# Performance work log

Measured on AMD Instinct MI355X. Metric: run time of the kernel, lower is better.

The kernel has to match this reference:

```python
import jax, jax.numpy as jnp
import numpy as np

N_NODES = 100000
N_EDGES = 1600000
D_IN = 64
D_HID = 64
D_ACT = 16


def gcn_conv(x, W, b, src, dst, n_nodes):
    """PyG-style GCNConv: D^-1/2 (A+I) D^-1/2 (x @ W) + b."""
    h = x @ W  # [N, out]
    ones = jnp.ones(src.shape[0], dtype=x.dtype)
    # degree with self-loops (in-degree + 1)
    deg = jax.ops.segment_sum(ones, dst, num_segments=n_nodes) + 1.0
    dinv = jax.lax.rsqrt(deg)  # [N]
    coef = dinv[src] * dinv[dst]  # [E]
    agg = jax.ops.segment_sum(h[src] * coef[:, None], dst, num_segments=n_nodes)
    agg = agg + h * (dinv * dinv)[:, None]  # self-loop term
    return agg + b


def setup_inputs() -> dict:
    key = jax.random.key(0)
    ks = jax.random.split(key, 6)
    x = jax.random.normal(ks[0], (N_NODES, D_IN), dtype=jnp.float32)
    edge_index = jax.random.randint(ks[1], (2, N_EDGES), 0, N_NODES, dtype=jnp.int64)
    s1 = 1.0 / np.sqrt(D_IN)
    s2 = 1.0 / np.sqrt(D_HID)
    W1 = jax.random.normal(ks[2], (D_IN, D_HID), dtype=jnp.float32) * s1
    b1 = jnp.zeros((D_HID,), dtype=jnp.float32)
    W2 = jax.random.normal(ks[3], (D_HID, D_HID), dtype=jnp.float32) * s2
    b2 = jnp.zeros((D_HID,), dtype=jnp.float32)
    Wfc = jax.random.normal(ks[4], (D_HID, D_ACT), dtype=jnp.float32) * s2
    bfc = jnp.zeros((D_ACT,), dtype=jnp.float32)
    return {"x": x, "edge_index": edge_index, "W1": W1, "b1": b1,
            "W2": W2, "b2": b2, "Wfc": Wfc, "bfc": bfc}


def reference(x, edge_index, W1, b1, W2, b2, Wfc, bfc):
    src, dst = edge_index[0], edge_index[1]
    n = x.shape[0]
    h = jax.nn.relu(gcn_conv(x, W1, b1, src, dst, n))
    h = jax.nn.relu(gcn_conv(h, W2, b2, src, dst, n))
    q_values = h @ Wfc + bfc
    return q_values
```

## Files before the change

### kernel.cpp

```cpp
#include <hip/hip_runtime.h>

#define NN 100000
#define NE 1600000
#define NCAP 64
#define NB2 782
#define NBP2 1024
#define CAP2 2560
#define CHUNK 2048
#define NCHUNK 782

typedef __attribute__((ext_vector_type(8))) short short8;
typedef __attribute__((ext_vector_type(4))) float f32x4;

static __device__ __forceinline__ unsigned short f2bf(float f) {
    unsigned u = __float_as_uint(f);
    u += 0x7fffu + ((u >> 16) & 1u);
    return (unsigned short)(u >> 16);
}
static __device__ __forceinline__ float bflo(unsigned u) { return __uint_as_float(u << 16); }
static __device__ __forceinline__ float bfhi(unsigned u) { return __uint_as_float(u & 0xffff0000u); }

static __device__ __forceinline__ short8 as_s8(uint4 u) {
    union { uint4 u4; short8 s8; } x; x.u4 = u; return x.s8;
}
static __device__ __forceinline__ f32x4 mfma16(short8 a, short8 b, f32x4 c) {
    return __builtin_amdgcn_mfma_f32_16x16x32_bf16(a, b, c, 0, 0, 0);
}

static __device__ __forceinline__ void split8(float4 a, float4 b, short8& hi8, short8& lo8) {
    float vv[8] = {a.x, a.y, a.z, a.w, b.x, b.y, b.z, b.w};
    unsigned h[8], l[8];
    #pragma unroll
    for (int j = 0; j < 8; ++j) {
        h[j] = f2bf(vv[j]);
        l[j] = f2bf(vv[j] - bflo(h[j]));
    }
    uint4 uh, ul;
    uh.x = h[0] | (h[1] << 16); uh.y = h[2] | (h[3] << 16);
    uh.z = h[4] | (h[5] << 16); uh.w = h[6] | (h[7] << 16);
    ul.x = l[0] | (l[1] << 16); ul.y = l[2] | (l[3] << 16);
    ul.z = l[4] | (l[5] << 16); ul.w = l[6] | (l[7] << 16);
    hi8 = as_s8(uh); lo8 = as_s8(ul);
}

__global__ void zero_gcur(int* __restrict__ p) {
    int t = blockIdx.x * blockDim.x + threadIdx.x;
    if (t < NBP2) p[t] = 0;
}

__global__ __launch_bounds__(256) void bin_edges(const int* __restrict__ src,
                                                 const int* __restrict__ dst,
                                                 int* __restrict__ gcur,
                                                 int* __restrict__ pairs) {
    __shared__ int lcnt[NBP2];
    __shared__ int lnext[NBP2];
    int t = threadIdx.x;
    #pragma unroll
    for (int i = 0; i < 4; ++i) lcnt[t + 256 * i] = 0;
    __syncthreads();
    int base = blockIdx.x * CHUNK;
    int end = min(base + CHUNK, NE);
    for (int e = base + t; e < end; e += 256) atomicAdd(&lcnt[dst[e] >> 7], 1);
    __syncthreads();
    #pragma unroll
    for (int i = 0; i < 4; ++i) {
        int b = t + 256 * i;
        int v = lcnt[b];
        if (v) lnext[b] = b * CAP2 + atomicAdd(&gcur[b], v);
    }
    __syncthreads();
    for (int e = base + t; e < end; e += 256) {
        int d = dst[e];
        int p = atomicAdd(&lnext[d >> 7], 1);
        pairs[p] = src[e] | ((d & 127) << 17);
    }
}

__global__ __launch_bounds__(256) void slab_place(const int* __restrict__ pairs,
                                                  const int* __restrict__ gcur,
                                                  int* __restrict__ esrc,
                                                  int* __restrict__ cnt,
                                                  float* __restrict__ dinv) {
    __shared__ int lc[128];
    int b = blockIdx.x;
    int t = threadIdx.x;
    if (t < 128) lc[t] = 0;
    __syncthreads();
    int e0 = b * CAP2;
    int e1 = e0 + min(gcur[b], CAP2);
    for (int i = e0 + t; i < e1; i += 256) {
        int w = pairs[i];
        int li = w >> 17;
        int p = atomicAdd(&lc[li], 1);
        if (p < NCAP) esrc[(((b << 7) + li) << 6) + p] = w & 0x1FFFF;
    }
    __syncthreads();
    if (t < 128) {
        int node = (b << 7) + t;
        if (node < NN) {
            int c = lc[t];
            cnt[node] = min(c, NCAP);
            dinv[node] = rsqrtf((float)c + 1.0f);
        }
    }
}

__global__ void wpack(const float* __restrict__ W1, const float* __restrict__ W2,
                      uint4* __restrict__ P) {
    int tid = blockIdx.x * blockDim.x + threadIdx.x;
    if (tid >= 1024) return;
    int w = tid >> 9;
    int f = tid & 511;
    int c = f >> 7;
    int t = (f >> 6) & 1;
    int lane = f & 63;
    const float* W = w ? W2 : W1;
    int k0 = t * 32 + (lane >> 4) * 8;
    int n  = c * 16 + (lane & 15);
    unsigned sh[8], sl[8];
    #pragma unroll
    for (int j = 0; j < 8; ++j) {
        float v = W[(k0 + j) * 64 + n];
        sh[j] = f2bf(v);
        sl[j] = f2bf(v - bflo(sh[j]));
    }
    uint4 ph, pl;
    ph.x = sh[0] | (sh[1] << 16); ph.y = sh[2] | (sh[3] << 16);
    ph.z = sh[4] | (sh[5] << 16); ph.w = sh[6] | (sh[7] << 16);
    pl.x = sl[0] | (sl[1] << 16); pl.y = sl[2] | (sl[3] << 16);
    pl.z = sl[4] | (sl[5] << 16); pl.w = sl[6] | (sl[7] << 16);
    P[w * 1024 + f]       = ph;
    P[w * 1024 + 512 + f] = pl;
}

__global__ __launch_bounds__(256) void gemm1_mfma(const float* __restrict__ X,
                                                  const uint4* __restrict__ WP,
                                                  const float* __restrict__ dinv,
                                                  uint4* __restrict__ G4) {
    __shared__ __align__(16) unsigned short Ls[4][16][64];
    int wave = threadIdx.x >> 6, lane = threadIdx.x & 63;
    int tile = blockIdx.x * 4 + wave;
    bool active = tile < (NN / 16);
    int node0 = (active ? tile : 0) * 16;
    int r = lane & 15, g = lane >> 4;

    const float* xr = X + (size_t)(node0 + r) * 64 + g * 8;
    float4 x0a = *(const float4*)(xr);
    float4 x0b = *(const float4*)(xr + 4);
    float4 x1a = *(const float4*)(xr + 32);
    float4 x1b = *(const float4*)(xr + 36);
    short8 ah0, al0, ah1, al1;
    split8(x0a, x0b, ah0, al0);
    split8(x1a, x1b, ah1, al1);

    f32x4 acc[4];
    #pragma unroll
    for (int c = 0; c < 4; ++c) acc[c] = (f32x4){0.f, 0.f, 0.f, 0.f};
    #pragma unroll
    for (int c = 0; c < 4; ++c) {
        short8 bh0 = as_s8(WP[(c * 2 + 0) * 64 + lane]);
        short8 bl0 = as_s8(WP[512 + (c * 2 + 0) * 64 + lane]);
        short8 bh1 = as_s8(WP[(c * 2 + 1) * 64 + lane]);
        short8 bl1 = as_s8(WP[512 + (c * 2 + 1) * 64 + lane]);
        acc[c] = mfma16(ah0, bh0, acc[c]);
        acc[c] = mfma16(al0, bh0, acc[c]);
        acc[c] = mfma16(ah0, bl0, acc[c]);
        acc[c] = mfma16(ah1, bh1, acc[c]);
        acc[c] = mfma16(al1, bh1, acc[c]);
        acc[c] = mfma16(ah1, bl1, acc[c]);
    }
    float dd[4];
    #pragma unroll
    for (int rr = 0; rr < 4; ++rr) dd[rr] = dinv[node0 + g * 4 + rr];
    #pragma unroll
    for (int c = 0; c < 4; ++c) {
        #pragma unroll
        for (int rr = 0; rr < 4; ++rr)
            Ls[wave][g * 4 + rr][c * 16 + r] = f2bf(acc[c][rr] * dd[rr]);
    }
    __syncthreads();
    if (active) {
        #pragma unroll
        for (int i = 0; i < 2; ++i) {
            int idx = lane + i * 64;
            int row = idx >> 3, u = idx & 7;
            G4[(size_t)(node0 + row) * 8 + u] = *(const uint4*)&Ls[wave][row][u * 8];
        }
    }
}

__global__ __launch_bounds__(256) void gemm2_mfma(const uint4* __restrict__ X4,
                                                  const uint4* __restrict__ WP,
                                                  const float* __restrict__ dinv,
                                                  uint4* __restrict__ G4) {
    __shared__ __align__(16) unsigned short Ls[4][16][64];
    int wave = threadIdx.x >> 6, lane = threadIdx.x & 63;
    int tile = blockIdx.x * 4 + wave;
    bool active = tile < (NN / 16);
    int node0 = (active ? tile : 0) * 16;
    int r = lane & 15, g = lane >> 4;

    short8 a0 = as_s8(X4[(size_t)(node0 + r) * 8 + g]);
    short8 a1 = as_s8(X4[(size_t)(node0 + r) * 8 + 4 + g]);

    f32x4 acc[4];
    #pragma unroll
    for (int c = 0; c < 4; ++c) acc[c] = (f32x4){0.f, 0.f, 0.f, 0.f};
    #pragma unroll
    for (int c = 0; c < 4; ++c) {
        short8 bh0 = as_s8(WP[(c * 2 + 0) * 64 + lane]);
        short8 bl0 = as_s8(WP[512 + (c * 2 + 0) * 64 + lane]);
        short8 bh1 = as_s8(WP[(c * 2 + 1) * 64 + lane]);
        short8 bl1 = as_s8(WP[512 + (c * 2 + 1) * 64 + lane]);
        acc[c] = mfma16(a0, bh0, acc[c]);
        acc[c] = mfma16(a0, bl0, acc[c]);
        acc[c] = mfma16(a1, bh1, acc[c]);
        acc[c] = mfma16(a1, bl1, acc[c]);
    }
    float dd[4];
    #pragma unroll
    for (int rr = 0; rr < 4; ++rr) dd[rr] = dinv[node0 + g * 4 + rr];
    #pragma unroll
    for (int c = 0; c < 4; ++c) {
        #pragma unroll
        for (int rr = 0; rr < 4; ++rr)
            Ls[wave][g * 4 + rr][c * 16 + r] = f2bf(acc[c][rr] * dd[rr]);
    }
    __syncthreads();
    if (active) {
        #pragma unroll
        for (int i = 0; i < 2; ++i) {
            int idx = lane + i * 64;
            int row = idx >> 3, u = idx & 7;
            G4[(size_t)(node0 + row) * 8 + u] = *(const uint4*)&Ls[wave][row][u * 8];
        }
    }
}

__global__ __launch_bounds__(256) void gather_bf16(
        const int* __restrict__ cnt, const int* __restrict__ esrc,
        const float* __restrict__ dinv, const uint4* __restrict__ G4,
        const float* __restrict__ b, uint4* __restrict__ outH) {
    int node = (int)((blockIdx.x * blockDim.x + threadIdx.x) >> 6);
    int lane = threadIdx.x & 63;
    int e = lane >> 3, m = lane & 7;
    int j0 = node << 6;
    int e1 = j0 + cnt[node];
    float a0 = 0.f, a1 = 0.f, a2 = 0.f, a3 = 0.f, a4 = 0.f, a5 = 0.f, a6 = 0.f, a7 = 0.f;
    int j = j0 + e;
    for (; j + 8 < e1; j += 16) {
        int s0 = esrc[j], s1 = esrc[j + 8];
        uint4 u0 = G4[s0 * 8 + m];
        uint4 u1 = G4[s1 * 8 + m];
        a0 += bflo(u0.x) + bflo(u1.x); a1 += bfhi(u0.x) + bfhi(u1.x);
        a2 += bflo(u0.y) + bflo(u1.y); a3 += bfhi(u0.y) + bfhi(u1.y);
        a4 += bflo(u0.z) + bflo(u1.z); a5 += bfhi(u0.z) + bfhi(u1.z);
        a6 += bflo(u0.w) + bflo(u1.w); a7 += bfhi(u0.w) + bfhi(u1.w);
    }
    for (; j < e1; j += 8) {
        uint4 u = G4[esrc[j] * 8 + m];
        a0 += bflo(u.x); a1 += bfhi(u.x); a2 += bflo(u.y); a3 += bfhi(u.y);
        a4 += bflo(u.z); a5 += bfhi(u.z); a6 += bflo(u.w); a7 += bfhi(u.w);
    }
    a0 += __shfl_xor(a0, 8);  a1 += __shfl_xor(a1, 8);  a2 += __shfl_xor(a2, 8);  a3 += __shfl_xor(a3, 8);
    a4 += __shfl_xor(a4, 8);  a5 += __shfl_xor(a5, 8);  a6 += __shfl_xor(a6, 8);  a7 += __shfl_xor(a7, 8);
    a0 += __shfl_xor(a0, 16); a1 += __shfl_xor(a1, 16); a2 += __shfl_xor(a2, 16); a3 += __shfl_xor(a3, 16);
    a4 += __shfl_xor(a4, 16); a5 += __shfl_xor(a5, 16); a6 += __shfl_xor(a6, 16); a7 += __shfl_xor(a7, 16);
    a0 += __shfl_xor(a0, 32); a1 += __shfl_xor(a1, 32); a2 += __shfl_xor(a2, 32); a3 += __shfl_xor(a3, 32);
    a4 += __shfl_xor(a4, 32); a5 += __shfl_xor(a5, 32); a6 += __shfl_xor(a6, 32); a7 += __shfl_xor(a7, 32);
    if (e == 0) {
        float dd = dinv[node];
        uint4 us = G4[node * 8 + m];
        a0 += bflo(us.x); a1 += bfhi(us.x); a2 += bflo(us.y); a3 += bfhi(us.y);
        a4 += bflo(us.z); a5 += bfhi(us.z); a6 += bflo(us.w); a7 += bfhi(us.w);
        float4 b0 = ((const float4*)b)[2 * m];
        float4 b1v = ((const float4*)b)[2 * m + 1];
        float h0 = fmaxf(fmaf(a0, dd, b0.x), 0.f);
        float h1 = fmaxf(fmaf(a1, dd, b0.y), 0.f);
        float h2 = fmaxf(fmaf(a2, dd, b0.z), 0.f);
        float h3 = fmaxf(fmaf(a3, dd, b0.w), 0.f);
        float h4 = fmaxf(fmaf(a4, dd, b1v.x), 0.f);
        float h5 = fmaxf(fmaf(a5, dd, b1v.y), 0.f);
        float h6 = fmaxf(fmaf(a6, dd, b1v.z), 0.f);
        float h7 = fmaxf(fmaf(a7, dd, b1v.w), 0.f);
        uint4 pk;
        pk.x = (unsigned)f2bf(h0) | ((unsigned)f2bf(h1) << 16);
        pk.y = (unsigned)f2bf(h2) | ((unsigned)f2bf(h3) << 16);
        pk.z = (unsigned)f2bf(h4) | ((unsigned)f2bf(h5) << 16);
        pk.w = (unsigned)f2bf(h6) | ((unsigned)f2bf(h7) << 16);
        outH[(size_t)node * 8 + m] = pk;
    }
}

__global__ __launch_bounds__(256) void gather_fc(
        const int* __restrict__ cnt, const int* __restrict__ esrc,
        const float* __restrict__ dinv, const uint4* __restrict__ G4,
        const float* __restrict__ b2, const float* __restrict__ Wfc,
        const float* __restrict__ bfc, float* __restrict__ out) {
    int tid = threadIdx.x;
    int w = tid >> 6, lane = tid & 63;
    int e = lane >> 3, m = lane & 7;
    int q = lane >> 4, c = lane & 15;
    int node = blockIdx.x * 4 + w;
    float Wreg[16];
    #pragma unroll
    for (int i = 0; i < 16; ++i) Wreg[i] = Wfc[(q * 16 + i) * 16 + c];
    int j0 = node << 6;
    int e1 = j0 + cnt[node];
    float a0 = 0.f, a1 = 0.f, a2 = 0.f, a3 = 0.f, a4 = 0.f, a5 = 0.f, a6 = 0.f, a7 = 0.f;
    int j = j0 + e;
    for (; j + 8 < e1; j += 16) {
        int s0 = esrc[j], s1 = esrc[j + 8];
        uint4 u0 = G4[s0 * 8 + m];
        uint4 u1 = G4[s1 * 8 + m];
        a0 += bflo(u0.x) + bflo(u1.x); a1 += bfhi(u0.x) + bfhi(u1.x);
        a2 += bflo(u0.y) + bflo(u1.y); a3 += bfhi(u0.y) + bfhi(u1.y);
        a4 += bflo(u0.z) + bflo(u1.z); a5 += bfhi(u0.z) + bfhi(u1.z);
        a6 += bflo(u0.w) + bflo(u1.w); a7 += bfhi(u0.w) + bfhi(u1.w);
    }
    for (; j < e1; j += 8) {
        uint4 u = G4[esrc[j] * 8 + m];
        a0 += bflo(u.x); a1 += bfhi(u.x); a2 += bflo(u.y); a3 += bfhi(u.y);
        a4 += bflo(u.z); a5 += bfhi(u.z); a6 += bflo(u.w); a7 += bfhi(u.w);
    }
    a0 += __shfl_xor(a0, 8);  a1 += __shfl_xor(a1, 8);  a2 += __shfl_xor(a2, 8);  a3 += __shfl_xor(a3, 8);
    a4 += __shfl_xor(a4, 8);  a5 += __shfl_xor(a5, 8);  a6 += __shfl_xor(a6, 8);  a7 += __shfl_xor(a7, 8);
    a0 += __shfl_xor(a0, 16); a1 += __shfl_xor(a1, 16); a2 += __shfl_xor(a2, 16); a3 += __shfl_xor(a3, 16);
    a4 += __shfl_xor(a4, 16); a5 += __shfl_xor(a5, 16); a6 += __shfl_xor(a6, 16); a7 += __shfl_xor(a7, 16);
    a0 += __shfl_xor(a0, 32); a1 += __shfl_xor(a1, 32); a2 += __shfl_xor(a2, 32); a3 += __shfl_xor(a3, 32);
    a4 += __shfl_xor(a4, 32); a5 += __shfl_xor(a5, 32); a6 += __shfl_xor(a6, 32); a7 += __shfl_xor(a7, 32);
    float dd = dinv[node];
    uint4 us = G4[node * 8 + m];
    a0 += bflo(us.x); a1 += bfhi(us.x); a2 += bflo(us.y); a3 += bfhi(us.y);
    a4 += bflo(us.z); a5 += bfhi(us.z); a6 += bflo(us.w); a7 += bfhi(us.w);
    float4 b0 = ((const float4*)b2)[2 * m];
    float4 b1v = ((const float4*)b2)[2 * m + 1];
    a0 = fmaxf(fmaf(a0, dd, b0.x), 0.f);
    a1 = fmaxf(fmaf(a1, dd, b0.y), 0.f);
    a2 = fmaxf(fmaf(a2, dd, b0.z), 0.f);
    a3 = fmaxf(fmaf(a3, dd, b0.w), 0.f);
    a4 = fmaxf(fmaf(a4, dd, b1v.x), 0.f);
    a5 = fmaxf(fmaf(a5, dd, b1v.y), 0.f);
    a6 = fmaxf(fmaf(a6, dd, b1v.z), 0.f);
    a7 = fmaxf(fmaf(a7, dd, b1v.w), 0.f);
    int sl0 = 2 * q, sl1 = 2 * q + 1;
    float acc = 0.f;
    acc = fmaf(__shfl(a0, sl0), Wreg[0], acc);
    acc = fmaf(__shfl(a1, sl0), Wreg[1], acc);
    acc = fmaf(__shfl(a2, sl0), Wreg[2], acc);
    acc = fmaf(__shfl(a3, sl0), Wreg[3], acc);
    acc = fmaf(__shfl(a4, sl0), Wreg[4], acc);
    acc = fmaf(__shfl(a5, sl0), Wreg[5], acc);
    acc = fmaf(__shfl(a6, sl0), Wreg[6], acc);
    acc = fmaf(__shfl(a7, sl0), Wreg[7], acc);
    acc = fmaf(__shfl(a0, sl1), Wreg[8], acc);
    acc = fmaf(__shfl(a1, sl1), Wreg[9], acc);
    acc = fmaf(__shfl(a2, sl1), Wreg[10], acc);
    acc = fmaf(__shfl(a3, sl1), Wreg[11], acc);
    acc = fmaf(__shfl(a4, sl1), Wreg[12], acc);
    acc = fmaf(__shfl(a5, sl1), Wreg[13], acc);
    acc = fmaf(__shfl(a6, sl1), Wreg[14], acc);
    acc = fmaf(__shfl(a7, sl1), Wreg[15], acc);
    acc += __shfl_xor(acc, 16);
    acc += __shfl_xor(acc, 32);
    if (lane < 16) out[node * 16 + c] = acc + bfc[c];
}

extern "C" void kernel_launch(void* const* d_in, const int* in_sizes, int n_in,
                              void* d_out, int out_size, void* d_ws, size_t ws_size,
                              hipStream_t stream) {
    const float* x   = (const float*)d_in[0];
    const int*   ei  = (const int*)d_in[1];
    const float* W1  = (const float*)d_in[2];
    const float* b1  = (const float*)d_in[3];
    const float* W2  = (const float*)d_in[4];
    const float* b2  = (const float*)d_in[5];
    const float* Wfc = (const float*)d_in[6];
    const float* bfc = (const float*)d_in[7];
    float* out = (float*)d_out;

    const int* src = ei;
    const int* dst = ei + NE;

    int*      gcur  = (int*)d_ws;
    int*      cnt   = gcur + NBP2;
    float*    dinvp = (float*)(cnt + NN);
    int*      esrc  = (int*)(dinvp + NN);
    unsigned* G     = (unsigned*)(esrc + (size_t)NN * NCAP);
    uint4*    bufB  = (uint4*)(G + (size_t)NN * 32);
    uint4*    WPK   = (uint4*)((unsigned*)bufB + (size_t)NN * 32);
    int*      pairs = (int*)bufB;

    zero_gcur<<<4, 256, 0, stream>>>(gcur);
    wpack<<<4, 256, 0, stream>>>(W1, W2, WPK);
    bin_edges<<<NCHUNK, 256, 0, stream>>>(src, dst, gcur, pairs);
    slab_place<<<NB2, 256, 0, stream>>>(pairs, gcur, esrc, cnt, dinvp);

    gemm1_mfma<<<(NN / 16 + 3) / 4, 256, 0, stream>>>(x, WPK, dinvp, (uint4*)G);
    gather_bf16<<<NN / 4, 256, 0, stream>>>(cnt, esrc, dinvp, (const uint4*)G, b1, bufB);

    gemm2_mfma<<<(NN / 16 + 3) / 4, 256, 0, stream>>>(bufB, WPK + 1024, dinvp, (uint4*)G);
    gather_fc<<<NN / 4, 256, 0, stream>>>(cnt, esrc, dinvp, (const uint4*)G, b2, Wfc, bfc, out);
}
```

Before: 249.7 us.

## Batch neighbor-index loads via shuffle, fuse gcur zeroing, register-cache edges in binning

The gather kernels now load all of a node's neighbor indices in one coalesced 64-lane read and broadcast them with shuffles. They then issue up to four (or eight) independent feature-row loads before accumulating, replacing the serial index-then-load loop and exposing more memory-level parallelism. Zeroing of the bin counters moves into the weight-packing kernel, which removes one launch. Binning keeps each thread's eight src/dst values in registers so the second pass does not re-read them from global memory. The costs are extra registers and predicated loads for low-degree nodes.

```diff
diff --git a/kernel.cpp b/kernel.cpp
--- a/kernel.cpp
+++ b/kernel.cpp
@@ -43,11 +43,6 @@
     hi8 = as_s8(uh); lo8 = as_s8(ul);
 }
 
-__global__ void zero_gcur(int* __restrict__ p) {
-    int t = blockIdx.x * blockDim.x + threadIdx.x;
-    if (t < NBP2) p[t] = 0;
-}
-
 __global__ __launch_bounds__(256) void bin_edges(const int* __restrict__ src,
                                                  const int* __restrict__ dst,
                                                  int* __restrict__ gcur,
@@ -59,8 +54,15 @@
     for (int i = 0; i < 4; ++i) lcnt[t + 256 * i] = 0;
     __syncthreads();
     int base = blockIdx.x * CHUNK;
-    int end = min(base + CHUNK, NE);
-    for (int e = base + t; e < end; e += 256) atomicAdd(&lcnt[dst[e] >> 7], 1);
+    int sr[8], dr[8];
+    #pragma unroll
+    for (int i = 0; i < 8; ++i) {
+        int e = base + t + 256 * i;
+        bool v = e < NE;
+        sr[i] = v ? src[e] : 0;
+        dr[i] = v ? dst[e] : -1;
+        if (v) atomicAdd(&lcnt[dr[i] >> 7], 1);
+    }
     __syncthreads();
     #pragma unroll
     for (int i = 0; i < 4; ++i) {
@@ -69,10 +71,12 @@
         if (v) lnext[b] = b * CAP2 + atomicAdd(&gcur[b], v);
     }
     __syncthreads();
-    for (int e = base + t; e < end; e += 256) {
-        int d = dst[e];
-        int p = atomicAdd(&lnext[d >> 7], 1);
-        pairs[p] = src[e] | ((d & 127) << 17);
+    #pragma unroll
+    for (int i = 0; i < 8; ++i) {
+        if (dr[i] >= 0) {
+            int p = atomicAdd(&lnext[dr[i] >> 7], 1);
+            pairs[p] = sr[i] | ((dr[i] & 127) << 17);
+        }
     }
 }
 
@@ -106,9 +110,10 @@
 }
 
 __global__ void wpack(const float* __restrict__ W1, const float* __restrict__ W2,
-                      uint4* __restrict__ P) {
+                      uint4* __restrict__ P, int* __restrict__ gcur) {
     int tid = blockIdx.x * blockDim.x + threadIdx.x;
     if (tid >= 1024) return;
+    gcur[tid] = 0;
     int w = tid >> 9;
     int f = tid & 511;
     int c = f >> 7;
@@ -237,37 +242,65 @@
     }
 }
 
+#define ACC8(u) do { \
+    a0 += bflo((u).x); a1 += bfhi((u).x); a2 += bflo((u).y); a3 += bfhi((u).y); \
+    a4 += bflo((u).z); a5 += bfhi((u).z); a6 += bflo((u).w); a7 += bfhi((u).w); } while (0)
+
+#define GATHER_CORE(node)                                                     \
+    int deg = cnt[node];                                                      \
+    int sidx = esrc[((node) << 6) + lane];                                    \
+    int nt = (deg - e + 7) >> 3;        \
+    int s0 = __shfl(sidx, e);                                                 \
+    int s1 = __shfl(sidx, e + 8);                                             \
+    int s2 = __shfl(sidx, e + 16);                                            \
+    int s3 = __shfl(sidx, e + 24);                                            \
+    float a0 = 0.f, a1 = 0.f, a2 = 0.f, a3 = 0.f,                             \
+          a4 = 0.f, a5 = 0.f, a6 = 0.f, a7 = 0.f;                             \
+    uint4 u0, u1, u2, u3;                                                     \
+    if (nt > 0) u0 = G4[s0 * 8 + m];                                          \
+    if (nt > 1) u1 = G4[s1 * 8 + m];                                          \
+    if (nt > 2) u2 = G4[s2 * 8 + m];                                          \
+    if (nt > 3) u3 = G4[s3 * 8 + m];                                          \
+    if (nt > 0) ACC8(u0);                                                     \
+    if (nt > 1) ACC8(u1);                                                     \
+    if (nt > 2) ACC8(u2);                                                     \
+    if (nt > 3) ACC8(u3);                                                     \
+    if (__any(nt > 4)) {                          \
+        int s4 = __shfl(sidx, e + 32);                                        \
+        int s5 = __shfl(sidx, e + 40);                                        \
+        int s6 = __shfl(sidx, e + 48);                                        \
+        int s7 = __shfl(sidx, e + 56);                                        \
+        uint4 u4, u5, u6, u7;                                                 \
+        if (nt > 4) u4 = G4[s4 * 8 + m];                                      \
+        if (nt > 5) u5 = G4[s5 * 8 + m];                                      \
+        if (nt > 6) u6 = G4[s6 * 8 + m];                                      \
+        if (nt > 7) u7 = G4[s7 * 8 + m];                                      \
+        if (nt > 4) ACC8(u4);                                                 \
+        if (nt > 5) ACC8(u5);                                                 \
+        if (nt > 6) ACC8(u6);                                                 \
+        if (nt > 7) ACC8(u7);                                                 \
+    }                                                                         \
+    a0 += __shfl_xor(a0, 8);  a1 += __shfl_xor(a1, 8);                        \
+    a2 += __shfl_xor(a2, 8);  a3 += __shfl_xor(a3, 8);                        \
+    a4 += __shfl_xor(a4, 8);  a5 += __shfl_xor(a5, 8);                        \
+    a6 += __shfl_xor(a6, 8);  a7 += __shfl_xor(a7, 8);                        \
+    a0 += __shfl_xor(a0, 16); a1 += __shfl_xor(a1, 16);                       \
+    a2 += __shfl_xor(a2, 16); a3 += __shfl_xor(a3, 16);                       \
+    a4 += __shfl_xor(a4, 16); a5 += __shfl_xor(a5, 16);                       \
+    a6 += __shfl_xor(a6, 16); a7 += __shfl_xor(a7, 16);                       \
+    a0 += __shfl_xor(a0, 32); a1 += __shfl_xor(a1, 32);                       \
+    a2 += __shfl_xor(a2, 32); a3 += __shfl_xor(a3, 32);                       \
+    a4 += __shfl_xor(a4, 32); a5 += __shfl_xor(a5, 32);                       \
+    a6 += __shfl_xor(a6, 32); a7 += __shfl_xor(a7, 32);
+
 __global__ __launch_bounds__(256) void gather_bf16(
         const int* __restrict__ cnt, const int* __restrict__ esrc,
         const float* __restrict__ dinv, const uint4* __restrict__ G4,
         const float* __restrict__ b, uint4* __restrict__ outH) {
-    int node = (int)((blockIdx.x * blockDim.x + threadIdx.x) >> 6);
+    int node = blockIdx.x * 4 + (threadIdx.x >> 6);
     int lane = threadIdx.x & 63;
     int e = lane >> 3, m = lane & 7;
-    int j0 = node << 6;
-    int e1 = j0 + cnt[node];
-    float a0 = 0.f, a1 = 0.f, a2 = 0.f, a3 = 0.f, a4 = 0.f, a5 = 0.f, a6 = 0.f, a7 = 0.f;
-    int j = j0 + e;
-    for (; j + 8 < e1; j += 16) {
-        int s0 = esrc[j], s1 = esrc[j + 8];
-        uint4 u0 = G4[s0 * 8 + m];
-        uint4 u1 = G4[s1 * 8 + m];
-        a0 += bflo(u0.x) + bflo(u1.x); a1 += bfhi(u0.x) + bfhi(u1.x);
-        a2 += bflo(u0.y) + bflo(u1.y); a3 += bfhi(u0.y) + bfhi(u1.y);
-        a4 += bflo(u0.z) + bflo(u1.z); a5 += bfhi(u0.z) + bfhi(u1.z);
-        a6 += bflo(u0.w) + bflo(u1.w); a7 += bfhi(u0.w) + bfhi(u1.w);
-    }
-    for (; j < e1; j += 8) {
-        uint4 u = G4[esrc[j] * 8 + m];
-        a0 += bflo(u.x); a1 += bfhi(u.x); a2 += bflo(u.y); a3 += bfhi(u.y);
-        a4 += bflo(u.z); a5 += bfhi(u.z); a6 += bflo(u.w); a7 += bfhi(u.w);
-    }
-    a0 += __shfl_xor(a0, 8);  a1 += __shfl_xor(a1, 8);  a2 += __shfl_xor(a2, 8);  a3 += __shfl_xor(a3, 8);
-    a4 += __shfl_xor(a4, 8);  a5 += __shfl_xor(a5, 8);  a6 += __shfl_xor(a6, 8);  a7 += __shfl_xor(a7, 8);
-    a0 += __shfl_xor(a0, 16); a1 += __shfl_xor(a1, 16); a2 += __shfl_xor(a2, 16); a3 += __shfl_xor(a3, 16);
-    a4 += __shfl_xor(a4, 16); a5 += __shfl_xor(a5, 16); a6 += __shfl_xor(a6, 16); a7 += __shfl_xor(a7, 16);
-    a0 += __shfl_xor(a0, 32); a1 += __shfl_xor(a1, 32); a2 += __shfl_xor(a2, 32); a3 += __shfl_xor(a3, 32);
-    a4 += __shfl_xor(a4, 32); a5 += __shfl_xor(a5, 32); a6 += __shfl_xor(a6, 32); a7 += __shfl_xor(a7, 32);
+    GATHER_CORE(node)
     if (e == 0) {
         float dd = dinv[node];
         uint4 us = G4[node * 8 + m];
@@ -297,38 +330,14 @@
         const float* __restrict__ dinv, const uint4* __restrict__ G4,
         const float* __restrict__ b2, const float* __restrict__ Wfc,
         const float* __restrict__ bfc, float* __restrict__ out) {
-    int tid = threadIdx.x;
-    int w = tid >> 6, lane = tid & 63;
+    int node = blockIdx.x * 4 + (threadIdx.x >> 6);
+    int lane = threadIdx.x & 63;
     int e = lane >> 3, m = lane & 7;
     int q = lane >> 4, c = lane & 15;
-    int node = blockIdx.x * 4 + w;
     float Wreg[16];
     #pragma unroll
     for (int i = 0; i < 16; ++i) Wreg[i] = Wfc[(q * 16 + i) * 16 + c];
-    int j0 = node << 6;
-    int e1 = j0 + cnt[node];
-    float a0 = 0.f, a1 = 0.f, a2 = 0.f, a3 = 0.f, a4 = 0.f, a5 = 0.f, a6 = 0.f, a7 = 0.f;
-    int j = j0 + e;
-    for (; j + 8 < e1; j += 16) {
-        int s0 = esrc[j], s1 = esrc[j + 8];
-        uint4 u0 = G4[s0 * 8 + m];
-        uint4 u1 = G4[s1 * 8 + m];
-        a0 += bflo(u0.x) + bflo(u1.x); a1 += bfhi(u0.x) + bfhi(u1.x);
-        a2 += bflo(u0.y) + bflo(u1.y); a3 += bfhi(u0.y) + bfhi(u1.y);
-        a4 += bflo(u0.z) + bflo(u1.z); a5 += bfhi(u0.z) + bfhi(u1.z);
-        a6 += bflo(u0.w) + bflo(u1.w); a7 += bfhi(u0.w) + bfhi(u1.w);
-    }
-    for (; j < e1; j += 8) {
-        uint4 u = G4[esrc[j] * 8 + m];
-        a0 += bflo(u.x); a1 += bfhi(u.x); a2 += bflo(u.y); a3 += bfhi(u.y);
-        a4 += bflo(u.z); a5 += bfhi(u.z); a6 += bflo(u.w); a7 += bfhi(u.w);
-    }
-    a0 += __shfl_xor(a0, 8);  a1 += __shfl_xor(a1, 8);  a2 += __shfl_xor(a2, 8);  a3 += __shfl_xor(a3, 8);
-    a4 += __shfl_xor(a4, 8);  a5 += __shfl_xor(a5, 8);  a6 += __shfl_xor(a6, 8);  a7 += __shfl_xor(a7, 8);
-    a0 += __shfl_xor(a0, 16); a1 += __shfl_xor(a1, 16); a2 += __shfl_xor(a2, 16); a3 += __shfl_xor(a3, 16);
-    a4 += __shfl_xor(a4, 16); a5 += __shfl_xor(a5, 16); a6 += __shfl_xor(a6, 16); a7 += __shfl_xor(a7, 16);
-    a0 += __shfl_xor(a0, 32); a1 += __shfl_xor(a1, 32); a2 += __shfl_xor(a2, 32); a3 += __shfl_xor(a3, 32);
-    a4 += __shfl_xor(a4, 32); a5 += __shfl_xor(a5, 32); a6 += __shfl_xor(a6, 32); a7 += __shfl_xor(a7, 32);
+    GATHER_CORE(node)
     float dd = dinv[node];
     uint4 us = G4[node * 8 + m];
     a0 += bflo(us.x); a1 += bfhi(us.x); a2 += bflo(us.y); a3 += bfhi(us.y);
@@ -391,8 +400,7 @@
     uint4*    WPK   = (uint4*)((unsigned*)bufB + (size_t)NN * 32);
     int*      pairs = (int*)bufB;
 
-    zero_gcur<<<4, 256, 0, stream>>>(gcur);
-    wpack<<<4, 256, 0, stream>>>(W1, W2, WPK);
+    wpack<<<4, 256, 0, stream>>>(W1, W2, WPK, gcur);
     bin_edges<<<NCHUNK, 256, 0, stream>>>(src, dst, gcur, pairs);
     slab_place<<<NB2, 256, 0, stream>>>(pairs, gcur, esrc, cnt, dinvp);
 
```

New measurement: 238.9 us. -4.3%, faster.
